# Performance work log

Hardware: AMD Instinct MI355X
Metric: run time of the kernel (lower is better)

Reference implementation:

```python
import jax, jax.numpy as jnp
import numpy as np

# ---- config constants (cfg) ----
AA, LP, Tc = 1.0, 1.0, 1.0
OMEGA_PHI, ALPHA_PHI, Lc = 1.0, 0.01, 1.0
CSE, CLE = 0.5, 0.00574
AC_PRE_SCALE = 1.0
AC1 = 2 * AA * LP * Tc
AC2 = LP * OMEGA_PHI * Tc
AC3 = LP * ALPHA_PHI * Tc / Lc**2

N, HID, NLAYERS, EMB = 65536, 128, 4, 64  # 2*EMB == HID


def setup_inputs() -> dict:
    key = jax.random.key(0)
    ks = jax.random.split(key, 6)
    x = jax.random.uniform(ks[0], (N, 2), dtype=jnp.float32)
    t = jax.random.uniform(ks[1], (N, 1), dtype=jnp.float32)
    B = jax.random.normal(ks[2], (3, EMB), dtype=jnp.float32)  # fourier features
    Wh = jax.random.normal(ks[3], (NLAYERS, HID, HID), dtype=jnp.float32) / np.sqrt(HID)
    bh = jnp.zeros((NLAYERS, HID), dtype=jnp.float32)
    Wout = jax.random.normal(ks[4], (HID, 2), dtype=jnp.float32) / np.sqrt(HID)
    bout = jnp.zeros((2,), dtype=jnp.float32)
    return {"x": x, "t": t, "B": B, "Wh": Wh, "bh": bh, "Wout": Wout, "bout": bout}


def reference(x, t, B, Wh, bh, Wout, bout):
    mirror = jnp.array([-1.0, 1.0], dtype=x.dtype)

    def mlp(xx, tt):  # xx:(2,), tt:(1,) -> (2,)
        z = jnp.concatenate([xx, tt])              # (3,)
        f = 2 * jnp.pi * (z @ B)                   # (EMB,)
        h = jnp.concatenate([jnp.sin(f), jnp.cos(f)])  # (HID,)
        def layer(h, wb):
            W, b = wb
            return jnp.tanh(h @ W + b), None
        h, _ = jax.lax.scan(layer, h, (Wh, bh))
        return h @ Wout + bout

    def net_u(xx, tt):  # hard-constrained (phi, c), symmetrized in x
        def hard_cons(xx_):
            phi, cl = jnp.tanh(mlp(xx_, tt)) / 2 + 0.5
            cl = cl * (1 - CSE + CLE)
            c = (CSE - CLE) * (-2 * phi**3 + 3 * phi**2) + cl
            return jnp.stack([phi, c])
        return (hard_cons(xx) + hard_cons(xx * mirror)) / 2

    def net_ac_point(xx, tt):  # Allen-Cahn residual at one collocation point
        phi, c = net_u(xx, tt)
        h_phi = -2 * phi**3 + 3 * phi**2
        dh_dphi = -6 * phi**2 + 6 * phi
        dg_dphi = 4 * phi**3 - 6 * phi**2 + 2 * phi
        dphi_dt = jax.jacrev(lambda t_: net_u(xx, t_)[0])(tt)          # (1,)
        hess = jax.hessian(lambda x_: net_u(x_, tt)[0])(xx)            # (2,2)
        nabla2phi = jnp.trace(hess)
        ac = (dphi_dt.squeeze()
              - AC1 * (c - h_phi * (CSE - CLE) - CLE) * (CSE - CLE) * dh_dphi
              + AC2 * dg_dphi
              - AC3 * nabla2phi)
        return ac / AC_PRE_SCALE

    return jax.vmap(net_ac_point)(x, t)  # (N,) PDE residuals
```

## Files before the change

### kernel.cpp

```cpp
#include <hip/hip_runtime.h>
#include <math.h>

#define PTS_PER_BLOCK 6
#define NPTS_PER_WAVE 3
#define WAVES_PER_BLOCK 2

typedef _Float16 h8 __attribute__((ext_vector_type(8)));
typedef _Float16 h2 __attribute__((ext_vector_type(2)));
typedef __fp16   fp16x2 __attribute__((ext_vector_type(2)));
typedef float    f4 __attribute__((ext_vector_type(4)));
typedef unsigned int uint32;

#define CSE_C 0.5f
#define CLE_C 0.00574f
#define DCOEF (CSE_C - CLE_C)
#define KCOEF (1.0f - CSE_C + CLE_C)

__device__ __forceinline__ float tanh_fast(float xx) {
    float e = __expf(2.0f * xx);
    float r = __builtin_amdgcn_rcpf(e + 1.0f);
    return fmaf(-2.0f, r, 1.0f);
}
__device__ __forceinline__ unsigned short f2h(float a) {
    union { _Float16 h; unsigned short u; } ua; ua.h = (_Float16)a; return ua.u;
}
__device__ __forceinline__ h2 pkrtz(float a, float b) {
    union { fp16x2 f; h2 h; } x; x.f = __builtin_amdgcn_cvt_pkrtz(a, b); return x.h;
}
__device__ __forceinline__ uint32 pk2h(float a, float b) {
    union { h2 h; uint32 u; } x; x.h = pkrtz(a, b); return x.u;
}
__device__ __forceinline__ h8 h8_from4(uint32 a, uint32 b, uint32 c, uint32 d) {
    union { uint32 u[4]; h8 v; } x; x.u[0] = a; x.u[1] = b; x.u[2] = c; x.u[3] = d;
    return x.v;
}

extern "C" __global__ __launch_bounds__(256)
void pinn_prep(const float* __restrict__ Wh, uint32* __restrict__ Wp)
{
    int gid  = blockIdx.x * 256 + threadIdx.x;
    int d    = gid & 3;
    int lane = (gid >> 2) & 63;
    int kt   = (gid >> 8) & 3;
    int jo   = (gid >> 10) & 7;
    int L    = gid >> 13;
    int j    = kt * 32 + (lane >> 4) * 8 + 2 * d;
    int jout = jo * 16 + (lane & 15);
    float w0 = Wh[(L * 128 + j) * 128 + jout];
    float w1 = Wh[(L * 128 + j + 1) * 128 + jout];
    Wp[gid] = pk2h(w0, w1);
}

extern "C" __global__ __launch_bounds__(128, 4)
void pinn_mfma(const float* __restrict__ x, const float* __restrict__ t,
               const float* __restrict__ B, const uint32* __restrict__ Wp,
               const float* __restrict__ bh, const float* __restrict__ Wout,
               const float* __restrict__ bout, float* __restrict__ out, int npts)
{
    __shared__ __align__(16) unsigned short H[WAVES_PER_BLOCK][32][136];

    const int tid  = threadIdx.x;
    const int lane = tid & 63;
    const int wv   = tid >> 6;
    const int c    = lane & 15;
    const int g    = lane >> 4;
    const int base_pt = blockIdx.x * PTS_PER_BLOCK + wv * NPTS_PER_WAVE;

    unsigned short* Hb = &H[wv][0][0];

    uint4 wt[2][4];
    {
        const uint4* W0 = (const uint4*)Wp;
        #pragma unroll
        for (int kt = 0; kt < 4; ++kt) wt[0][kt] = W0[kt * 64 + lane];
        #pragma unroll
        for (int kt = 0; kt < 4; ++kt) wt[1][kt] = W0[(4 + kt) * 64 + lane];
    }

    {
        const float TWO_PI = 6.28318530717958647692f;
        const float Br0 = B[lane], Br1 = B[64 + lane], Br2 = B[128 + lane];
        const float b0 = TWO_PI * Br0, b1 = TWO_PI * Br1, b2 = TWO_PI * Br2;
        const float bsq = fmaf(b0, b0, b1 * b1);
        #pragma unroll
        for (int pl = 0; pl < 3; ++pl) {
            int pt = base_pt + pl; if (pt > npts - 1) pt = npts - 1;
            const float2 xx = *(const float2*)&x[2 * pt];
            const float tt = t[pt];
            const float uc = fmaf(xx.y, Br1, tt * Br2);
            const float ux = xx.x * Br0;
            #pragma unroll
            for (int mir = 0; mir < 2; ++mir) {
                float u = mir ? (uc - ux) : (uc + ux);
                float r = u - floorf(u);
                float sf = __builtin_amdgcn_sinf(r);
                float cf = __builtin_amdgcn_cosf(r);
                const int b  = pl * 2 + mir;
                const int rs = (b < 3) ? 5 * b : 16 + 5 * (b - 3);
                Hb[(rs + 0) * 136 + lane] = f2h(sf);
                Hb[(rs + 1) * 136 + lane] = f2h(cf * b2);
                Hb[(rs + 2) * 136 + lane] = f2h(cf * b0);
                Hb[(rs + 3) * 136 + lane] = f2h(cf * b1);
                Hb[(rs + 4) * 136 + lane] = f2h(-sf * bsq);
                Hb[(rs + 0) * 136 + 64 + lane] = f2h(cf);
                Hb[(rs + 1) * 136 + 64 + lane] = f2h(-sf * b2);
                Hb[(rs + 2) * 136 + 64 + lane] = f2h(-sf * b0);
                Hb[(rs + 3) * 136 + 64 + lane] = f2h(-sf * b1);
                Hb[(rs + 4) * 136 + 64 + lane] = f2h(-cf * bsq);
            }
        }
    }
    asm volatile("s_waitcnt lgkmcnt(0)" ::: "memory");

    for (int L = 0; L < 4; ++L) {
        h8 bf[2][4];
        #pragma unroll
        for (int ct = 0; ct < 2; ++ct)
            #pragma unroll
            for (int kt = 0; kt < 4; ++kt)
                bf[ct][kt] = *(const h8*)&Hb[(ct * 16 + c) * 136 + kt * 32 + g * 8];

        const uint4* WL = (const uint4*)Wp + (size_t)L * 2048;
        const uint4* WN = WL + 2048;

        #pragma unroll
        for (int jo = 0; jo < 8; ++jo) {
            const int cur = jo & 1;
            f4 a0 = {0.f, 0.f, 0.f, 0.f}, a1 = {0.f, 0.f, 0.f, 0.f};
            #pragma unroll
            for (int kt = 0; kt < 4; ++kt) {
                union { uint4 u; h8 v; } af;
                af.u = wt[cur][kt];
                a0 = __builtin_amdgcn_mfma_f32_16x16x32_f16(af.v, bf[0][kt], a0, 0, 0, 0);
                a1 = __builtin_amdgcn_mfma_f32_16x16x32_f16(af.v, bf[1][kt], a1, 0, 0, 0);
            }
            if (jo < 6) {
                #pragma unroll
                for (int kt = 0; kt < 4; ++kt)
                    wt[cur][kt] = WL[((jo + 2) * 4 + kt) * 64 + lane];
            } else if (L < 3) {
                #pragma unroll
                for (int kt = 0; kt < 4; ++kt)
                    wt[cur][kt] = WN[((jo - 6) * 4 + kt) * 64 + lane];
            }
            union { h2 h[2]; uint2 u; } w0, w1;
            w0.h[0] = pkrtz(a0[0], a0[1]); w0.h[1] = pkrtz(a0[2], a0[3]);
            w1.h[0] = pkrtz(a1[0], a1[1]); w1.h[1] = pkrtz(a1[2], a1[3]);
            *(uint2*)&Hb[(0  + c) * 136 + jo * 16 + g * 4] = w0.u;
            *(uint2*)&Hb[(16 + c) * 136 + jo * 16 + g * 4] = w1.u;
        }
        asm volatile("s_waitcnt lgkmcnt(0)" ::: "memory");

        {
            const int jb = 2 * lane;
            const float2 bj = *(const float2*)&bh[L * 128 + jb];
            const h2 bias2 = pkrtz(bj.x, bj.y);
            const h2 m2 = {(_Float16)(-2.0f), (_Float16)(-2.0f)};
            #pragma unroll
            for (int b = 0; b < 6; ++b) {
                int rs = (b < 3) ? 5 * b : 16 + 5 * (b - 3);
                h2 vp = *(const h2*)&Hb[(rs + 0) * 136 + jb];
                h2 tp = *(const h2*)&Hb[(rs + 1) * 136 + jb];
                h2 pp = *(const h2*)&Hb[(rs + 2) * 136 + jb];
                h2 qp = *(const h2*)&Hb[(rs + 3) * 136 + jb];
                h2 Lp = *(const h2*)&Hb[(rs + 4) * 136 + jb];
                vp = vp + bias2;
                float y0 = tanh_fast((float)vp[0]);
                float y1 = tanh_fast((float)vp[1]);
                h2 yp = pkrtz(y0, y1);
                h2 sp = pkrtz(fmaf(-y0, y0, 1.f), fmaf(-y1, y1, 1.f));
                h2 qq = __builtin_elementwise_fma(pp, pp, qp * qp);
                h2 Ln = sp * __builtin_elementwise_fma(yp * m2, qq, Lp);
                *(h2*)&Hb[(rs + 0) * 136 + jb] = yp;
                *(h2*)&Hb[(rs + 1) * 136 + jb] = sp * tp;
                *(h2*)&Hb[(rs + 2) * 136 + jb] = sp * pp;
                *(h2*)&Hb[(rs + 3) * 136 + jb] = sp * qp;
                *(h2*)&Hb[(rs + 4) * 136 + jb] = Ln;
            }
        }
        asm volatile("s_waitcnt lgkmcnt(0)" ::: "memory");
    }

    {
        h8 afo[4];
        const int   mc  = c & 1;
        const float sel = (c < 2) ? 1.0f : 0.0f;
        #pragma unroll
        for (int kt = 0; kt < 4; ++kt) {
            uint32 u[4];
            #pragma unroll
            for (int d = 0; d < 4; ++d) {
                int k = kt * 32 + g * 8 + 2 * d;
                float w0 = Wout[k * 2 + mc] * sel;
                float w1 = Wout[(k + 1) * 2 + mc] * sel;
                u[d] = pk2h(w0, w1);
            }
            afo[kt] = h8_from4(u[0], u[1], u[2], u[3]);
        }
        h8 bfo[2][4];
        #pragma unroll
        for (int ct = 0; ct < 2; ++ct)
            #pragma unroll
            for (int kt = 0; kt < 4; ++kt)
                bfo[ct][kt] = *(const h8*)&Hb[(ct * 16 + c) * 136 + kt * 32 + g * 8];

        f4 ac0 = {0.f, 0.f, 0.f, 0.f}, ac1 = {0.f, 0.f, 0.f, 0.f};
        #pragma unroll
        for (int kt = 0; kt < 4; ++kt) {
            ac0 = __builtin_amdgcn_mfma_f32_16x16x32_f16(afo[kt], bfo[0][kt], ac0, 0, 0, 0);
            ac1 = __builtin_amdgcn_mfma_f32_16x16x32_f16(afo[kt], bfo[1][kt], ac1, 0, 0, 0);
        }
        float* S = (float*)Hb;
        if (g == 0) {
            f4 pack = {ac0[0], ac0[1], ac1[0], ac1[1]};
            *(f4*)&S[c * 4] = pack;
        }
        asm volatile("s_waitcnt lgkmcnt(0)" ::: "memory");

        if (lane < 3) {
            int pt = base_pt + lane;
            if (pt < npts) {
                float bo0 = bout[0], bo1 = bout[1];
                float ph = 0.f, cv = 0.f, ptd = 0.f, lp = 0.f;
                #pragma unroll
                for (int br = 0; br < 2; ++br) {
                    int b  = 2 * lane + br;
                    int ct = (b < 3) ? 0 : 1;
                    int cc = ((b < 3) ? b : b - 3) * 5;
                    float o0v = S[(cc + 0) * 4 + 2 * ct] + bo0;
                    float o0t = S[(cc + 1) * 4 + 2 * ct];
                    float o0p = S[(cc + 2) * 4 + 2 * ct];
                    float o0q = S[(cc + 3) * 4 + 2 * ct];
                    float o0L = S[(cc + 4) * 4 + 2 * ct];
                    float o1v = S[(cc + 0) * 4 + 2 * ct + 1] + bo1;
                    float T = tanh_fast(o0v);
                    float p = fmaf(0.5f, T, 0.5f);
                    float s = 0.5f * fmaf(-T, T, 1.f);
                    float lap = s * o0L - 2.f * T * s * fmaf(o0p, o0p, o0q * o0q);
                    float cl = KCOEF * fmaf(0.5f, tanh_fast(o1v), 0.5f);
                    float cb = fmaf(DCOEF, (-2.f * p + 3.f) * p * p, cl);
                    ph  += 0.5f * p;
                    cv  += 0.5f * cb;
                    ptd += 0.5f * s * o0t;
                    lp  += 0.5f * lap;
                }
                float hph = (-2.f * ph + 3.f) * ph * ph;
                float dh  = 6.f * ph * (1.f - ph);
                float dg  = ((4.f * ph - 6.f) * ph + 2.f) * ph;
                float ac  = ptd
                          - 2.f * ((cv - hph * DCOEF - CLE_C) * DCOEF) * dh
                          + dg
                          - 0.01f * lp;
                out[pt] = ac;
            }
        }
    }
}

extern "C" void kernel_launch(void* const* d_in, const int* in_sizes, int n_in,
                              void* d_out, int out_size, void* d_ws, size_t ws_size,
                              hipStream_t stream) {
    const float* x    = (const float*)d_in[0];
    const float* t    = (const float*)d_in[1];
    const float* B    = (const float*)d_in[2];
    const float* Wh   = (const float*)d_in[3];
    const float* bh   = (const float*)d_in[4];
    const float* Wout = (const float*)d_in[5];
    const float* bout = (const float*)d_in[6];
    float* out = (float*)d_out;
    uint32* Wp = (uint32*)d_ws;

    const int npts = in_sizes[0] / 2;
    hipLaunchKernelGGL(pinn_prep, dim3(128), dim3(256), 0, stream, Wh, Wp);
    const int nb = (npts + PTS_PER_BLOCK - 1) / PTS_PER_BLOCK;
    hipLaunchKernelGGL(pinn_mfma, dim3(nb), dim3(128), 0, stream,
                       x, t, B, Wp, bh, Wout, bout, out, npts);
}
```

Baseline: 137.0 us.

## Process six points per wave with four MFMA column tiles per weight fragment

Each wave now handles six collocation points (12 mirrored branches packed into 64 LDS rows) instead of three, and blocks shrink to a single wave. Each loaded weight fragment now feeds four MFMAs instead of two, which halves global weight traffic per point and amortizes the per-wave weight stream. In exchange it raises register pressure (more B fragments and accumulators) and LDS per wave, and the launch bound drops to 2 waves per EU, which may reduce latency hiding.

```diff
diff --git a/kernel.cpp b/kernel.cpp
--- a/kernel.cpp
+++ b/kernel.cpp
@@ -1,9 +1,7 @@
 #include <hip/hip_runtime.h>
 #include <math.h>
 
-#define PTS_PER_BLOCK 6
-#define NPTS_PER_WAVE 3
-#define WAVES_PER_BLOCK 2
+#define NPTS_PER_WAVE 6
 
 typedef _Float16 h8 __attribute__((ext_vector_type(8)));
 typedef _Float16 h2 __attribute__((ext_vector_type(2)));
@@ -51,22 +49,20 @@
     Wp[gid] = pk2h(w0, w1);
 }
 
-extern "C" __global__ __launch_bounds__(128, 4)
+extern "C" __global__ __launch_bounds__(64, 2)
 void pinn_mfma(const float* __restrict__ x, const float* __restrict__ t,
                const float* __restrict__ B, const uint32* __restrict__ Wp,
                const float* __restrict__ bh, const float* __restrict__ Wout,
                const float* __restrict__ bout, float* __restrict__ out, int npts)
 {
-    __shared__ __align__(16) unsigned short H[WAVES_PER_BLOCK][32][136];
-
-    const int tid  = threadIdx.x;
-    const int lane = tid & 63;
-    const int wv   = tid >> 6;
+    __shared__ __align__(16) unsigned short H[64][136];
+
+    const int lane = threadIdx.x;
     const int c    = lane & 15;
     const int g    = lane >> 4;
-    const int base_pt = blockIdx.x * PTS_PER_BLOCK + wv * NPTS_PER_WAVE;
-
-    unsigned short* Hb = &H[wv][0][0];
+    const int base_pt = blockIdx.x * NPTS_PER_WAVE;
+
+    unsigned short* Hb = &H[0][0];
 
     uint4 wt[2][4];
     {
@@ -83,7 +79,7 @@
         const float b0 = TWO_PI * Br0, b1 = TWO_PI * Br1, b2 = TWO_PI * Br2;
         const float bsq = fmaf(b0, b0, b1 * b1);
         #pragma unroll
-        for (int pl = 0; pl < 3; ++pl) {
+        for (int pl = 0; pl < 6; ++pl) {
             int pt = base_pt + pl; if (pt > npts - 1) pt = npts - 1;
             const float2 xx = *(const float2*)&x[2 * pt];
             const float tt = t[pt];
@@ -96,7 +92,7 @@
                 float sf = __builtin_amdgcn_sinf(r);
                 float cf = __builtin_amdgcn_cosf(r);
                 const int b  = pl * 2 + mir;
-                const int rs = (b < 3) ? 5 * b : 16 + 5 * (b - 3);
+                const int rs = (b / 3) * 16 + (b % 3) * 5;
                 Hb[(rs + 0) * 136 + lane] = f2h(sf);
                 Hb[(rs + 1) * 136 + lane] = f2h(cf * b2);
                 Hb[(rs + 2) * 136 + lane] = f2h(cf * b0);
@@ -113,9 +109,9 @@
     asm volatile("s_waitcnt lgkmcnt(0)" ::: "memory");
 
     for (int L = 0; L < 4; ++L) {
-        h8 bf[2][4];
-        #pragma unroll
-        for (int ct = 0; ct < 2; ++ct)
+        h8 bf[4][4];
+        #pragma unroll
+        for (int ct = 0; ct < 4; ++ct)
             #pragma unroll
             for (int kt = 0; kt < 4; ++kt)
                 bf[ct][kt] = *(const h8*)&Hb[(ct * 16 + c) * 136 + kt * 32 + g * 8];
@@ -127,12 +123,15 @@
         for (int jo = 0; jo < 8; ++jo) {
             const int cur = jo & 1;
             f4 a0 = {0.f, 0.f, 0.f, 0.f}, a1 = {0.f, 0.f, 0.f, 0.f};
+            f4 a2 = {0.f, 0.f, 0.f, 0.f}, a3 = {0.f, 0.f, 0.f, 0.f};
             #pragma unroll
             for (int kt = 0; kt < 4; ++kt) {
                 union { uint4 u; h8 v; } af;
                 af.u = wt[cur][kt];
                 a0 = __builtin_amdgcn_mfma_f32_16x16x32_f16(af.v, bf[0][kt], a0, 0, 0, 0);
                 a1 = __builtin_amdgcn_mfma_f32_16x16x32_f16(af.v, bf[1][kt], a1, 0, 0, 0);
+                a2 = __builtin_amdgcn_mfma_f32_16x16x32_f16(af.v, bf[2][kt], a2, 0, 0, 0);
+                a3 = __builtin_amdgcn_mfma_f32_16x16x32_f16(af.v, bf[3][kt], a3, 0, 0, 0);
             }
             if (jo < 6) {
                 #pragma unroll
@@ -143,11 +142,15 @@
                 for (int kt = 0; kt < 4; ++kt)
                     wt[cur][kt] = WN[((jo - 6) * 4 + kt) * 64 + lane];
             }
-            union { h2 h[2]; uint2 u; } w0, w1;
+            union { h2 h[2]; uint2 u; } w0, w1, w2, w3;
             w0.h[0] = pkrtz(a0[0], a0[1]); w0.h[1] = pkrtz(a0[2], a0[3]);
             w1.h[0] = pkrtz(a1[0], a1[1]); w1.h[1] = pkrtz(a1[2], a1[3]);
+            w2.h[0] = pkrtz(a2[0], a2[1]); w2.h[1] = pkrtz(a2[2], a2[3]);
+            w3.h[0] = pkrtz(a3[0], a3[1]); w3.h[1] = pkrtz(a3[2], a3[3]);
             *(uint2*)&Hb[(0  + c) * 136 + jo * 16 + g * 4] = w0.u;
             *(uint2*)&Hb[(16 + c) * 136 + jo * 16 + g * 4] = w1.u;
+            *(uint2*)&Hb[(32 + c) * 136 + jo * 16 + g * 4] = w2.u;
+            *(uint2*)&Hb[(48 + c) * 136 + jo * 16 + g * 4] = w3.u;
         }
         asm volatile("s_waitcnt lgkmcnt(0)" ::: "memory");
 
@@ -157,8 +160,8 @@
             const h2 bias2 = pkrtz(bj.x, bj.y);
             const h2 m2 = {(_Float16)(-2.0f), (_Float16)(-2.0f)};
             #pragma unroll
-            for (int b = 0; b < 6; ++b) {
-                int rs = (b < 3) ? 5 * b : 16 + 5 * (b - 3);
+            for (int b = 0; b < 12; ++b) {
+                const int rs = (b / 3) * 16 + (b % 3) * 5;
                 h2 vp = *(const h2*)&Hb[(rs + 0) * 136 + jb];
                 h2 tp = *(const h2*)&Hb[(rs + 1) * 136 + jb];
                 h2 pp = *(const h2*)&Hb[(rs + 2) * 136 + jb];
@@ -197,42 +200,49 @@
             }
             afo[kt] = h8_from4(u[0], u[1], u[2], u[3]);
         }
-        h8 bfo[2][4];
-        #pragma unroll
-        for (int ct = 0; ct < 2; ++ct)
+        h8 bfo[4][4];
+        #pragma unroll
+        for (int ct = 0; ct < 4; ++ct)
             #pragma unroll
             for (int kt = 0; kt < 4; ++kt)
                 bfo[ct][kt] = *(const h8*)&Hb[(ct * 16 + c) * 136 + kt * 32 + g * 8];
 
-        f4 ac0 = {0.f, 0.f, 0.f, 0.f}, ac1 = {0.f, 0.f, 0.f, 0.f};
+        f4 ac0 = {0.f,0.f,0.f,0.f}, ac1 = {0.f,0.f,0.f,0.f};
+        f4 ac2 = {0.f,0.f,0.f,0.f}, ac3 = {0.f,0.f,0.f,0.f};
         #pragma unroll
         for (int kt = 0; kt < 4; ++kt) {
             ac0 = __builtin_amdgcn_mfma_f32_16x16x32_f16(afo[kt], bfo[0][kt], ac0, 0, 0, 0);
             ac1 = __builtin_amdgcn_mfma_f32_16x16x32_f16(afo[kt], bfo[1][kt], ac1, 0, 0, 0);
+            ac2 = __builtin_amdgcn_mfma_f32_16x16x32_f16(afo[kt], bfo[2][kt], ac2, 0, 0, 0);
+            ac3 = __builtin_amdgcn_mfma_f32_16x16x32_f16(afo[kt], bfo[3][kt], ac3, 0, 0, 0);
         }
         float* S = (float*)Hb;
         if (g == 0) {
-            f4 pack = {ac0[0], ac0[1], ac1[0], ac1[1]};
-            *(f4*)&S[c * 4] = pack;
+            f4 p0 = {ac0[0], ac0[1], ac1[0], ac1[1]};
+            f4 p1 = {ac2[0], ac2[1], ac3[0], ac3[1]};
+            *(f4*)&S[c * 4]      = p0;
+            *(f4*)&S[64 + c * 4] = p1;
         }
         asm volatile("s_waitcnt lgkmcnt(0)" ::: "memory");
 
-        if (lane < 3) {
+        if (lane < 6) {
             int pt = base_pt + lane;
             if (pt < npts) {
                 float bo0 = bout[0], bo1 = bout[1];
                 float ph = 0.f, cv = 0.f, ptd = 0.f, lp = 0.f;
                 #pragma unroll
                 for (int br = 0; br < 2; ++br) {
-                    int b  = 2 * lane + br;
-                    int ct = (b < 3) ? 0 : 1;
-                    int cc = ((b < 3) ? b : b - 3) * 5;
-                    float o0v = S[(cc + 0) * 4 + 2 * ct] + bo0;
-                    float o0t = S[(cc + 1) * 4 + 2 * ct];
-                    float o0p = S[(cc + 2) * 4 + 2 * ct];
-                    float o0q = S[(cc + 3) * 4 + 2 * ct];
-                    float o0L = S[(cc + 4) * 4 + 2 * ct];
-                    float o1v = S[(cc + 0) * 4 + 2 * ct + 1] + bo1;
+                    int b    = 2 * lane + br;
+                    int ct   = b / 3;
+                    int cc   = (b % 3) * 5;
+                    int base = (ct >> 1) * 64;
+                    int half = 2 * (ct & 1);
+                    float o0v = S[base + (cc + 0) * 4 + half] + bo0;
+                    float o0t = S[base + (cc + 1) * 4 + half];
+                    float o0p = S[base + (cc + 2) * 4 + half];
+                    float o0q = S[base + (cc + 3) * 4 + half];
+                    float o0L = S[base + (cc + 4) * 4 + half];
+                    float o1v = S[base + (cc + 0) * 4 + half + 1] + bo1;
                     float T = tanh_fast(o0v);
                     float p = fmaf(0.5f, T, 0.5f);
                     float s = 0.5f * fmaf(-T, T, 1.f);
@@ -272,7 +282,7 @@
 
     const int npts = in_sizes[0] / 2;
     hipLaunchKernelGGL(pinn_prep, dim3(128), dim3(256), 0, stream, Wh, Wp);
-    const int nb = (npts + PTS_PER_BLOCK - 1) / PTS_PER_BLOCK;
-    hipLaunchKernelGGL(pinn_mfma, dim3(nb), dim3(128), 0, stream,
+    const int nb = (npts + NPTS_PER_WAVE - 1) / NPTS_PER_WAVE;
+    hipLaunchKernelGGL(pinn_mfma, dim3(nb), dim3(64), 0, stream,
                        x, t, B, Wp, bh, Wout, bout, out, npts);
 }
```

After: 127.6 us. 6.9% less time.
